# Performance work log

Measured on AMD Instinct MI355X. Metric: run time of the kernel, lower is better.

The kernel has to match this reference:

```python
import jax, jax.numpy as jnp
import numpy as np
import math

DIM = 1024
N_HEADS = 16
HEAD_DIM = DIM // N_HEADS
MAX_LEN = 4096
THETA = 10000.0
LN_EPS = 1e-5


def _rope_tables(dim, max_len, theta=THETA):
    # matches precompute_rope: freqs over even indices, angles = outer(t, freqs)
    inv = 1.0 / theta ** (np.arange(0, dim, 2, dtype=np.float32) / dim)
    t = np.arange(max_len, dtype=np.float32)
    ang = np.outer(t, inv)  # [max_len, dim//2]
    return jnp.asarray(np.cos(ang)), jnp.asarray(np.sin(ang))


def setup_inputs() -> dict:
    key = jax.random.key(0)
    ks = jax.random.split(key, 5)
    B, T, D = 2, 2048, DIM
    s = 1.0 / math.sqrt(D)
    x = jax.random.normal(ks[0], (B, T, D), dtype=jnp.float32)
    wq = jax.random.normal(ks[1], (D, D), dtype=jnp.float32) * s
    wk = jax.random.normal(ks[2], (D, D), dtype=jnp.float32) * s
    wv = jax.random.normal(ks[3], (D, D), dtype=jnp.float32) * s
    wo = jax.random.normal(ks[4], (D, D), dtype=jnp.float32) * s
    ln_g = jnp.ones((D,), dtype=jnp.float32)
    ln_b = jnp.zeros((D,), dtype=jnp.float32)
    cos, sin = _rope_tables(HEAD_DIM, MAX_LEN)
    return {"x": x, "wq": wq, "wk": wk, "wv": wv, "wo": wo,
            "ln_g": ln_g, "ln_b": ln_b, "cos": cos, "sin": sin}


def _rotate(x, cos, sin):
    # x: [B, T, H, hd]; complex multiply on interleaved (even, odd) pairs
    B, T, H, hd = x.shape
    xr = x.reshape(B, T, H, hd // 2, 2)
    x0, x1 = xr[..., 0], xr[..., 1]
    c = cos[None, :T, None, :]
    s = sin[None, :T, None, :]
    o0 = x0 * c - x1 * s
    o1 = x0 * s + x1 * c
    return jnp.stack([o0, o1], axis=-1).reshape(B, T, H, hd)


def reference(x, wq, wk, wv, wo, ln_g, ln_b, cos, sin):
    B, T, D = x.shape
    H, hd = N_HEADS, HEAD_DIM
    # LayerNorm
    mu = jnp.mean(x, axis=-1, keepdims=True)
    var = jnp.var(x, axis=-1, keepdims=True)
    h = (x - mu) * jax.lax.rsqrt(var + LN_EPS) * ln_g + ln_b
    # QKV projections (torch Linear: h @ W.T)
    q = jnp.einsum('btd,ed->bte', h, wq).reshape(B, T, H, hd)
    k = jnp.einsum('btd,ed->bte', h, wk).reshape(B, T, H, hd)
    v = jnp.einsum('btd,ed->bte', h, wv).reshape(B, T, H, hd)
    q = _rotate(q, cos, sin)
    k = _rotate(k, cos, sin)
    # full (non-causal) attention, scores [B, H, T, T]
    scores = jnp.einsum('bqhd,bkhd->bhqk', q, k) / math.sqrt(hd)
    attn = jax.nn.softmax(scores, axis=-1)
    out = jnp.einsum('bhqk,bkhd->bqhd', attn, v).reshape(B, T, D)
    return jnp.einsum('btd,ed->bte', out, wo)
```

## Files before the change

kernel.cpp:

```cpp
#include <hip/hip_runtime.h>
#include <hip/hip_bf16.h>

typedef __attribute__((ext_vector_type(4))) float          fx4;
typedef __attribute__((ext_vector_type(8))) __bf16         bfx8;
typedef __attribute__((ext_vector_type(8))) unsigned short usx8;
typedef __attribute__((ext_vector_type(4))) unsigned short usx4;

#define TLEN 2048
#define ROWS 4096
#define D    1024

__device__ __forceinline__ float bf2f(unsigned short u) {
    union { unsigned int i; float f; } v; v.i = ((unsigned int)u) << 16; return v.f;
}
__device__ __forceinline__ unsigned short f2bf(float f) {
    union { float f; unsigned int i; } v; v.f = f;
    unsigned int r = v.i + 0x7fffu + ((v.i >> 16) & 1u);
    return (unsigned short)(r >> 16);
}
__device__ __forceinline__ unsigned int cvtpk_bf16(float lo, float hi) {
    unsigned int r;
    asm("v_cvt_pk_bf16_f32 %0, %1, %2" : "=v"(r) : "v"(lo), "v"(hi));
    return r;
}
__device__ __forceinline__ void gload_lds16(const unsigned short* g, unsigned short* l) {
    __builtin_amdgcn_global_load_lds((const __attribute__((address_space(1))) void*)g,
                                     (__attribute__((address_space(3))) void*)l, 16, 0, 0);
}

__device__ __forceinline__ usx4 cvt4(fx4 a) {
    usx4 o;
    #pragma unroll
    for (int j = 0; j < 4; j++) o[j] = f2bf(a[j]);
    return o;
}
__global__ __launch_bounds__(256) void prep_kernel(const float* __restrict__ x,
                                                   const float* __restrict__ g,
                                                   const float* __restrict__ bta,
                                                   const float* __restrict__ wq, const float* __restrict__ wk,
                                                   const float* __restrict__ wv, const float* __restrict__ wo,
                                                   unsigned short* __restrict__ hout,
                                                   unsigned short* __restrict__ wqkv,
                                                   unsigned short* __restrict__ wob,
                                                   float* __restrict__ ropeTab) {
    const int tid = threadIdx.x;
    if (blockIdx.x >= 5120) {
        const int idx = (blockIdx.x - 5120) * 256 + tid;
        const int pi_ = idx >> 11, t = idx & 2047;
        float inv = __builtin_amdgcn_exp2f(-0.415241011861f * (float)pi_);
        float ang = (float)t * inv;
        ropeTab[idx * 2]     = cosf(ang);
        ropeTab[idx * 2 + 1] = sinf(ang);
        return;
    }
    if (blockIdx.x >= 4096) {
        const int i = (blockIdx.x - 4096) * 256 + tid;
        ((usx4*)wqkv)[i]          = cvt4(((const fx4*)wq)[i]);
        ((usx4*)wqkv)[262144 + i] = cvt4(((const fx4*)wk)[i]);
        ((usx4*)wqkv)[524288 + i] = cvt4(((const fx4*)wv)[i]);
        ((usx4*)wob)[i]           = cvt4(((const fx4*)wo)[i]);
        return;
    }
    const int row = blockIdx.x;
    fx4 v = ((const fx4*)(x + (size_t)row * D))[tid];
    float s  = v[0] + v[1] + v[2] + v[3];
    float s2 = v[0]*v[0] + v[1]*v[1] + v[2]*v[2] + v[3]*v[3];
    #pragma unroll
    for (int mk = 32; mk >= 1; mk >>= 1) { s += __shfl_xor(s, mk); s2 += __shfl_xor(s2, mk); }
    __shared__ float red[8];
    const int wave = tid >> 6, lane = tid & 63;
    if (lane == 0) { red[wave] = s; red[4 + wave] = s2; }
    __syncthreads();
    s  = red[0] + red[1] + red[2] + red[3];
    s2 = red[4] + red[5] + red[6] + red[7];
    float mu   = s * (1.0f / D);
    float var  = s2 * (1.0f / D) - mu * mu;
    float rstd = rsqrtf(var + 1e-5f);
    fx4 gv = ((const fx4*)g)[tid];
    fx4 bv = ((const fx4*)bta)[tid];
    usx4 o;
    #pragma unroll
    for (int j = 0; j < 4; j++) o[j] = f2bf((v[j] - mu) * rstd * gv[j] + bv[j]);
    ((usx4*)hout)[(size_t)row * 256 + tid] = o;
}

__global__ __launch_bounds__(512) void qkvt_gemm(const unsigned short* __restrict__ hbuf,
                                                 const unsigned short* __restrict__ wqkv,
                                                 unsigned short* __restrict__ qkout,
                                                 unsigned short* __restrict__ vtout,
                                                 const float* __restrict__ ropeTab) {
    constexpr int K = 1024;
    __shared__ __align__(16) unsigned short As[2][256 * 64];
    __shared__ __align__(16) unsigned short Bs[2][256 * 64];
    const int tid = threadIdx.x, lane = tid & 63, wave = tid >> 6;
    const int fr = lane & 15, fq = lane >> 4;
    const int wr = wave >> 2, wc = wave & 3;

    const int id = blockIdx.x;
    const bool isqk = id < 128;
    int bm, bn;
    const unsigned short *Ab, *Bb;
    if (isqk) {
        bm = id & 15; bn = id >> 4;
        Ab = hbuf + (size_t)(bm * 256) * K;
        Bb = wqkv + (size_t)(bn * 256) * K;
    } else {
        int j = id - 128; bm = j & 3; bn = j >> 2;
        Ab = wqkv + (size_t)(2048 * 1024) + (size_t)(bm * 256) * K;
        Bb = hbuf + (size_t)(bn * 256) * K;
    }

    const int srow   = wave * 8 + (lane >> 3);
    const int sc_dst = (lane & 7) * 8;
    const int sc_src = ((lane & 7) ^ (lane >> 3)) * 8;

    #define STAGE_Q(BUF, KT)                                                          \
        {                                                                             \
            _Pragma("unroll")                                                         \
            for (int i = 0; i < 4; i++) {                                             \
                const int r = srow + 64 * i;                                          \
                gload_lds16(Ab + (size_t)r * K + (KT) + sc_src, &As[BUF][r * 64 + sc_dst]); \
                gload_lds16(Bb + (size_t)r * K + (KT) + sc_src, &Bs[BUF][r * 64 + sc_dst]); \
            }                                                                         \
        }

    fx4 acc[8][4];
    #pragma unroll
    for (int m = 0; m < 8; m++)
        #pragma unroll
        for (int n = 0; n < 4; n++) acc[m][n] = (fx4)0.0f;

    STAGE_Q(0, 0)

    for (int kt = 0; kt < K; kt += 64) {
        const int b = (kt >> 6) & 1;
        __syncthreads();
        if (kt + 64 < K) STAGE_Q(b ^ 1, kt + 64)
        #pragma unroll
        for (int s = 0; s < 2; s++) {
            bfx8 aF[8], bF[4];
            #pragma unroll
            for (int m = 0; m < 8; m++)
                aF[m] = *(const bfx8*)&As[b][(wr * 128 + m * 16 + fr) * 64 + (((s * 4 + fq) ^ (fr & 7)) * 8)];
            #pragma unroll
            for (int n = 0; n < 4; n++)
                bF[n] = *(const bfx8*)&Bs[b][(wc * 64 + n * 16 + fr) * 64 + (((s * 4 + fq) ^ (fr & 7)) * 8)];
            #pragma unroll
            for (int m = 0; m < 8; m++)
                #pragma unroll
                for (int n = 0; n < 4; n++)
                    acc[m][n] = __builtin_amdgcn_mfma_f32_16x16x32_bf16(aF[m], bF[n], acc[m][n], 0, 0, 0);
        }
    }
    #undef STAGE_Q

    const int row0 = bm * 256 + wr * 128 + fq * 4;
    const int col0 = bn * 256 + wc * 64 + fr;
    if (isqk) {
        const float QS = 0.125f * 1.44269504088896f;
        const bool isq = bn < 4;
        const float sgn = (fr & 1) ? 1.0f : -1.0f;
        #pragma unroll
        for (int m = 0; m < 8; m++) {
            const int rbase = row0 + m * 16;
            const int tb = rbase & (TLEN - 1);
            #pragma unroll
            for (int n = 0; n < 4; n++) {
                const float* tp = ropeTab + ((((n * 8 + (fr >> 1)) << 11) | tb) << 1);
                fx4 csA = *(const fx4*)tp;
                fx4 csB = *(const fx4*)(tp + 4);
                #pragma unroll
                for (int j = 0; j < 4; j++) {
                    float c  = (j < 2) ? csA[2 * j]     : csB[2 * (j - 2)];
                    float s_ = (j < 2) ? csA[2 * j + 1] : csB[2 * (j - 2) + 1];
                    float self = acc[m][n][j];
                    float other = __shfl_xor(self, 1);
                    float o = self * c + other * (sgn * s_);
                    if (isq) o *= QS;
                    qkout[(size_t)(rbase + j) * 2048 + col0 + n * 16] = f2bf(o);
                }
            }
        }
    } else {
        const int bb = bn >> 3;
        #pragma unroll
        for (int m = 0; m < 8; m++)
            #pragma unroll
            for (int n = 0; n < 4; n++) {
                const int t = (col0 + n * 16) & (TLEN - 1);
                const int tp = (t & ~63) | ((n >> 1) * 32 + ((fr >> 2)) * 8 + ((n & 1)) * 4 + (fr & 3));
                #pragma unroll
                for (int j = 0; j < 4; j++) {
                    const int d = row0 + m * 16 + j;
                    vtout[(((size_t)(bb * 16 + (d >> 6)) * 64) + (d & 63)) * TLEN + tp] = f2bf(acc[m][n][j]);
                }
            }
    }
}

__global__ __launch_bounds__(256) void gemm_out64(const unsigned short* __restrict__ A,
                                                  const unsigned short* __restrict__ B,
                                                  float* __restrict__ C) {
    constexpr int K = 1024;
    __shared__ __align__(16) unsigned short As[128 * 64];
    __shared__ __align__(16) unsigned short Bs[64 * 64];
    const int tid = threadIdx.x, lane = tid & 63, wave = tid >> 6;
    const int fr = lane & 15, fq = lane >> 4;
    const int bm = blockIdx.x, bn = blockIdx.y;
    const int wr = wave >> 1, wc = wave & 1;

    const int srow   = wave * 8 + (lane >> 3);
    const int sc_dst = (lane & 7) * 8;
    const int sc_src = ((lane & 7) ^ (lane >> 3)) * 8;
    const unsigned short* Ab = A + (size_t)(bm * 128) * K;
    const unsigned short* Bb = B + (size_t)(bn * 64) * K;

    fx4 acc[4][2];
    #pragma unroll
    for (int m = 0; m < 4; m++)
        #pragma unroll
        for (int n = 0; n < 2; n++) acc[m][n] = (fx4)0.0f;

    for (int kt = 0; kt < K; kt += 64) {
        #pragma unroll
        for (int i = 0; i < 4; i++) {
            const int r = srow + 32 * i;
            gload_lds16(Ab + (size_t)r * K + kt + sc_src, &As[r * 64 + sc_dst]);
            if (i < 2)
                gload_lds16(Bb + (size_t)r * K + kt + sc_src, &Bs[r * 64 + sc_dst]);
        }
        __syncthreads();
        #pragma unroll
        for (int s = 0; s < 2; s++) {
            bfx8 aF[4], bF[2];
            #pragma unroll
            for (int m = 0; m < 4; m++)
                aF[m] = *(const bfx8*)&As[(wr * 64 + m * 16 + fr) * 64 + (((s * 4 + fq) ^ (fr & 7)) * 8)];
            #pragma unroll
            for (int n = 0; n < 2; n++)
                bF[n] = *(const bfx8*)&Bs[(wc * 32 + n * 16 + fr) * 64 + (((s * 4 + fq) ^ (fr & 7)) * 8)];
            #pragma unroll
            for (int m = 0; m < 4; m++)
                #pragma unroll
                for (int n = 0; n < 2; n++)
                    acc[m][n] = __builtin_amdgcn_mfma_f32_16x16x32_bf16(aF[m], bF[n], acc[m][n], 0, 0, 0);
        }
        __syncthreads();
    }

    const int row0 = bm * 128 + wr * 64 + fq * 4;
    const int col0 = bn * 64 + wc * 32 + fr;
    #pragma unroll
    for (int m = 0; m < 4; m++)
        #pragma unroll
        for (int n = 0; n < 2; n++)
            #pragma unroll
            for (int j = 0; j < 4; j++)
                C[(size_t)(row0 + m * 16 + j) * 1024 + col0 + n * 16] = acc[m][n][j];
}

__global__ __launch_bounds__(512) void attn_kernel(const unsigned short* __restrict__ qk,
                                                   const unsigned short* __restrict__ vt,
                                                   unsigned short* __restrict__ ao) {
    const int flat = blockIdx.x + (blockIdx.y << 3);
    const int sid  = (flat & 7) * 32 + (flat >> 3);
    const int qt = sid & 7, bh = sid >> 3;
    const int b = bh >> 4, hh = bh & 15;
    const int tid = threadIdx.x, lane = tid & 63, wave = tid >> 6;
    const int fr = lane & 15, fq = lane >> 4;

    __shared__ __align__(16) unsigned short sK[2][64 * 64];
    __shared__ __align__(16) unsigned short sVt[2][64 * 64];

    const size_t rs = 2048;
    const unsigned short* qb  = qk + (size_t)b * TLEN * rs + hh * 64;
    const unsigned short* kb  = qb + 1024;
    const unsigned short* vtb = vt + (size_t)bh * (64 * TLEN);

    bfx8 qF[2][2];
    #pragma unroll
    for (int g = 0; g < 2; g++) {
        int qrow = qt * 256 + wave * 32 + g * 16 + fr;
        const unsigned short* qp = qb + (size_t)qrow * rs + fq * 8;
        qF[g][0] = *(const bfx8*)qp;
        qF[g][1] = *(const bfx8*)(qp + 32);
    }
    union { unsigned short us[8]; bfx8 bf; } ones_u;
    #pragma unroll
    for (int i = 0; i < 8; i++) ones_u.us[i] = 0x3F80;

    const int srow = lane >> 3;
    const int scol = ((lane & 7) ^ srow) * 8;

    gload_lds16(kb  + (size_t)(wave * 8 + srow) * rs + scol,   &sK[0][wave * 512 + lane * 8]);
    gload_lds16(vtb + (size_t)(wave * 8 + srow) * TLEN + scol, &sVt[0][wave * 512 + lane * 8]);

    fx4 oacc[2][4];
    fx4 oextra[2] = {(fx4)0.0f, (fx4)0.0f};
    #pragma unroll
    for (int g = 0; g < 2; g++)
        #pragma unroll
        for (int db = 0; db < 4; db++) oacc[g][db] = (fx4)0.0f;

    #pragma unroll 2
    for (int t = 0; t < 32; ++t) {
        const int buf = t & 1;
        __syncthreads();

        if (t + 1 < 32) {
            const int kt = (t + 1) * 64;
            gload_lds16(kb  + (size_t)(kt + wave * 8 + srow) * rs + scol,
                        &sK[buf ^ 1][wave * 512 + lane * 8]);
            gload_lds16(vtb + (size_t)(wave * 8 + srow) * TLEN + kt + scol,
                        &sVt[buf ^ 1][wave * 512 + lane * 8]);
        }

        bfx8 kF[2][4];
        #pragma unroll
        for (int s = 0; s < 2; s++)
            #pragma unroll
            for (int n = 0; n < 4; n++)
                kF[s][n] = *(const bfx8*)&sK[buf][(n * 16 + fr) * 64 + (((s * 4 + fq) ^ (fr & 7)) * 8)];
        fx4 sacc0[4], sacc1[4];
        #pragma unroll
        for (int n = 0; n < 4; n++) { sacc0[n] = (fx4)0.0f; sacc1[n] = (fx4)0.0f; }
        __builtin_amdgcn_s_setprio(1);
        #pragma unroll
        for (int s = 0; s < 2; s++)
            #pragma unroll
            for (int n = 0; n < 4; n++)
                sacc0[n] = __builtin_amdgcn_mfma_f32_16x16x32_bf16(kF[s][n], qF[0][s], sacc0[n], 0, 0, 0);
        #pragma unroll
        for (int s = 0; s < 2; s++)
            #pragma unroll
            for (int n = 0; n < 4; n++)
                sacc1[n] = __builtin_amdgcn_mfma_f32_16x16x32_bf16(kF[s][n], qF[1][s], sacc1[n], 0, 0, 0);
        __builtin_amdgcn_s_setprio(0);

        unsigned int u0[4][2], u1[4][2];
        #pragma unroll
        for (int n = 0; n < 4; n++) {
            u0[n][0] = cvtpk_bf16(__builtin_amdgcn_exp2f(sacc0[n][0]), __builtin_amdgcn_exp2f(sacc0[n][1]));
            u0[n][1] = cvtpk_bf16(__builtin_amdgcn_exp2f(sacc0[n][2]), __builtin_amdgcn_exp2f(sacc0[n][3]));
        }

        bfx8 vF[2][4];
        #pragma unroll
        for (int s = 0; s < 2; s++)
            #pragma unroll
            for (int db = 0; db < 4; db++)
                vF[s][db] = *(const bfx8*)&sVt[buf][(db * 16 + fr) * 64 + (((s * 4 + fq) ^ (fr & 7)) * 8)];

        __builtin_amdgcn_s_setprio(1);
        #pragma unroll
        for (int s = 0; s < 2; s++) {
            union { unsigned int ui[4]; bfx8 bf; } cv;
            cv.ui[0] = u0[2 * s][0];     cv.ui[1] = u0[2 * s][1];
            cv.ui[2] = u0[2 * s + 1][0]; cv.ui[3] = u0[2 * s + 1][1];
            #pragma unroll
            for (int db = 0; db < 4; db++)
                oacc[0][db] = __builtin_amdgcn_mfma_f32_16x16x32_bf16(vF[s][db], cv.bf, oacc[0][db], 0, 0, 0);
            oextra[0] = __builtin_amdgcn_mfma_f32_16x16x32_bf16(ones_u.bf, cv.bf, oextra[0], 0, 0, 0);
        }
        __builtin_amdgcn_s_setprio(0);

        #pragma unroll
        for (int n = 0; n < 4; n++) {
            u1[n][0] = cvtpk_bf16(__builtin_amdgcn_exp2f(sacc1[n][0]), __builtin_amdgcn_exp2f(sacc1[n][1]));
            u1[n][1] = cvtpk_bf16(__builtin_amdgcn_exp2f(sacc1[n][2]), __builtin_amdgcn_exp2f(sacc1[n][3]));
        }

        __builtin_amdgcn_s_setprio(1);
        #pragma unroll
        for (int s = 0; s < 2; s++) {
            union { unsigned int ui[4]; bfx8 bf; } cv;
            cv.ui[0] = u1[2 * s][0];     cv.ui[1] = u1[2 * s][1];
            cv.ui[2] = u1[2 * s + 1][0]; cv.ui[3] = u1[2 * s + 1][1];
            #pragma unroll
            for (int db = 0; db < 4; db++)
                oacc[1][db] = __builtin_amdgcn_mfma_f32_16x16x32_bf16(vF[s][db], cv.bf, oacc[1][db], 0, 0, 0);
            oextra[1] = __builtin_amdgcn_mfma_f32_16x16x32_bf16(ones_u.bf, cv.bf, oextra[1], 0, 0, 0);
        }
        __builtin_amdgcn_s_setprio(0);
    }

    #pragma unroll
    for (int g = 0; g < 2; g++) {
        float invl = 1.0f / oextra[g][0];
        const int qrow = qt * 256 + wave * 32 + g * 16 + fr;
        unsigned short* aop = ao + (size_t)(b * TLEN + qrow) * 1024 + hh * 64 + fq * 4;
        #pragma unroll
        for (int db = 0; db < 4; db++) {
            usx4 o4;
            #pragma unroll
            for (int j = 0; j < 4; j++) o4[j] = f2bf(oacc[g][db][j] * invl);
            *(usx4*)(aop + db * 16) = o4;
        }
    }
}

extern "C" void kernel_launch(void* const* d_in, const int* in_sizes, int n_in,
                              void* d_out, int out_size, void* d_ws, size_t ws_size,
                              hipStream_t stream) {
    const float* x    = (const float*)d_in[0];
    const float* wq   = (const float*)d_in[1];
    const float* wk   = (const float*)d_in[2];
    const float* wv   = (const float*)d_in[3];
    const float* wo   = (const float*)d_in[4];
    const float* lng  = (const float*)d_in[5];
    const float* lnb  = (const float*)d_in[6];

    char* ws = (char*)d_ws;
    unsigned short* wob  = (unsigned short*)(ws);
    unsigned short* wqkv = (unsigned short*)(ws + (2u  << 20));
    unsigned short* hbuf = (unsigned short*)(ws + (8u  << 20));
    unsigned short* qk   = (unsigned short*)(ws + (16u << 20));
    unsigned short* vtb  = (unsigned short*)(ws + (32u << 20));
    unsigned short* ao   = (unsigned short*)(ws + (8u  << 20));
    float* ropeTab = (float*)d_out;

    prep_kernel<<<5632, 256, 0, stream>>>(x, lng, lnb, wq, wk, wv, wo, hbuf, wqkv, wob, ropeTab);
    qkvt_gemm<<<192, 512, 0, stream>>>(hbuf, wqkv, qk, vtb, ropeTab);
    attn_kernel<<<dim3(8, 32), 512, 0, stream>>>(qk, vtb, ao);
    gemm_out64<<<dim3(32, 16), 256, 0, stream>>>(ao, wob, (float*)d_out);
}
```

Baseline: 114.3 us.

## Load QKV GEMM B fragments from global and double attention KV tile size

In the QKV GEMM, the B operand is no longer staged through shared memory. Each wave loads its B fragments directly from global memory into registers, which halves LDS use and the staging traffic. The attention kernel now processes 128 keys per iteration instead of 64, with larger shared buffers, and interleaves K fragment loads with the MFMAs. This halves the number of barriers and loop iterations. The risks are uncoalesced, higher-latency global reads for B that are not covered by prefetching, and higher register and LDS pressure in attention.

```diff
diff --git a/kernel.cpp b/kernel.cpp
--- a/kernel.cpp
+++ b/kernel.cpp
@@ -91,7 +91,6 @@
                                                  const float* __restrict__ ropeTab) {
     constexpr int K = 1024;
     __shared__ __align__(16) unsigned short As[2][256 * 64];
-    __shared__ __align__(16) unsigned short Bs[2][256 * 64];
     const int tid = threadIdx.x, lane = tid & 63, wave = tid >> 6;
     const int fr = lane & 15, fq = lane >> 4;
     const int wr = wave >> 2, wc = wave & 3;
@@ -113,14 +112,14 @@
     const int srow   = wave * 8 + (lane >> 3);
     const int sc_dst = (lane & 7) * 8;
     const int sc_src = ((lane & 7) ^ (lane >> 3)) * 8;
-
-    #define STAGE_Q(BUF, KT)                                                          \
+    const unsigned short* Bfrag = Bb + (size_t)(wc * 64 + fr) * K + fq * 8;
+
+    #define STAGE_A(BUF, KT)                                                          \
         {                                                                             \
             _Pragma("unroll")                                                         \
             for (int i = 0; i < 4; i++) {                                             \
                 const int r = srow + 64 * i;                                          \
                 gload_lds16(Ab + (size_t)r * K + (KT) + sc_src, &As[BUF][r * 64 + sc_dst]); \
-                gload_lds16(Bb + (size_t)r * K + (KT) + sc_src, &Bs[BUF][r * 64 + sc_dst]); \
             }                                                                         \
         }
 
@@ -130,29 +129,33 @@
         #pragma unroll
         for (int n = 0; n < 4; n++) acc[m][n] = (fx4)0.0f;
 
-    STAGE_Q(0, 0)
-
+    STAGE_A(0, 0)
+
+    #pragma unroll 2
     for (int kt = 0; kt < K; kt += 64) {
         const int b = (kt >> 6) & 1;
         __syncthreads();
-        if (kt + 64 < K) STAGE_Q(b ^ 1, kt + 64)
+        if (kt + 64 < K) STAGE_A(b ^ 1, kt + 64)
+        bfx8 bF[2][4];
+        #pragma unroll
+        for (int s = 0; s < 2; s++)
+            #pragma unroll
+            for (int n = 0; n < 4; n++)
+                bF[s][n] = *(const bfx8*)(Bfrag + (size_t)(n * 16) * K + kt + s * 32);
         #pragma unroll
         for (int s = 0; s < 2; s++) {
-            bfx8 aF[8], bF[4];
+            bfx8 aF[8];
             #pragma unroll
             for (int m = 0; m < 8; m++)
                 aF[m] = *(const bfx8*)&As[b][(wr * 128 + m * 16 + fr) * 64 + (((s * 4 + fq) ^ (fr & 7)) * 8)];
-            #pragma unroll
-            for (int n = 0; n < 4; n++)
-                bF[n] = *(const bfx8*)&Bs[b][(wc * 64 + n * 16 + fr) * 64 + (((s * 4 + fq) ^ (fr & 7)) * 8)];
             #pragma unroll
             for (int m = 0; m < 8; m++)
                 #pragma unroll
                 for (int n = 0; n < 4; n++)
-                    acc[m][n] = __builtin_amdgcn_mfma_f32_16x16x32_bf16(aF[m], bF[n], acc[m][n], 0, 0, 0);
-        }
-    }
-    #undef STAGE_Q
+                    acc[m][n] = __builtin_amdgcn_mfma_f32_16x16x32_bf16(aF[m], bF[s][n], acc[m][n], 0, 0, 0);
+        }
+    }
+    #undef STAGE_A
 
     const int row0 = bm * 256 + wr * 128 + fq * 4;
     const int col0 = bn * 256 + wc * 64 + fr;
@@ -269,8 +272,8 @@
     const int tid = threadIdx.x, lane = tid & 63, wave = tid >> 6;
     const int fr = lane & 15, fq = lane >> 4;
 
-    __shared__ __align__(16) unsigned short sK[2][64 * 64];
-    __shared__ __align__(16) unsigned short sVt[2][64 * 64];
+    __shared__ __align__(16) unsigned short sK[2][128 * 64];
+    __shared__ __align__(16) unsigned short sVt[2][2 * 64 * 64];
 
     const size_t rs = 2048;
     const unsigned short* qb  = qk + (size_t)b * TLEN * rs + hh * 64;
@@ -292,8 +295,20 @@
     const int srow = lane >> 3;
     const int scol = ((lane & 7) ^ srow) * 8;
 
-    gload_lds16(kb  + (size_t)(wave * 8 + srow) * rs + scol,   &sK[0][wave * 512 + lane * 8]);
-    gload_lds16(vtb + (size_t)(wave * 8 + srow) * TLEN + scol, &sVt[0][wave * 512 + lane * 8]);
+    #define STAGE_ATTN(BUF, KT)                                                          \
+        {                                                                                \
+            _Pragma("unroll")                                                            \
+            for (int i = 0; i < 2; i++) {                                                \
+                const int rg = wave * 2 + i;                                             \
+                gload_lds16(kb + (size_t)((KT) + rg * 8 + srow) * rs + scol,             \
+                            &sK[BUF][rg * 512 + lane * 8]);                              \
+                const int sub = rg >> 3, drow = (rg & 7) * 8 + srow;                     \
+                gload_lds16(vtb + (size_t)drow * TLEN + (KT) + sub * 64 + scol,          \
+                            &sVt[BUF][rg * 512 + lane * 8]);                             \
+            }                                                                            \
+        }
+
+    STAGE_ATTN(0, 0)
 
     fx4 oacc[2][4];
     fx4 oextra[2] = {(fx4)0.0f, (fx4)0.0f};
@@ -303,86 +318,72 @@
         for (int db = 0; db < 4; db++) oacc[g][db] = (fx4)0.0f;
 
     #pragma unroll 2
-    for (int t = 0; t < 32; ++t) {
+    for (int t = 0; t < 16; ++t) {
         const int buf = t & 1;
         __syncthreads();
 
-        if (t + 1 < 32) {
-            const int kt = (t + 1) * 64;
-            gload_lds16(kb  + (size_t)(kt + wave * 8 + srow) * rs + scol,
-                        &sK[buf ^ 1][wave * 512 + lane * 8]);
-            gload_lds16(vtb + (size_t)(wave * 8 + srow) * TLEN + kt + scol,
-                        &sVt[buf ^ 1][wave * 512 + lane * 8]);
-        }
-
-        bfx8 kF[2][4];
+        if (t + 1 < 16) STAGE_ATTN(buf ^ 1, (t + 1) * 128)
+
+        fx4 s0[8], s1[8];
+        #pragma unroll
+        for (int n = 0; n < 8; n++) { s0[n] = (fx4)0.0f; s1[n] = (fx4)0.0f; }
+        __builtin_amdgcn_s_setprio(1);
         #pragma unroll
         for (int s = 0; s < 2; s++)
             #pragma unroll
-            for (int n = 0; n < 4; n++)
-                kF[s][n] = *(const bfx8*)&sK[buf][(n * 16 + fr) * 64 + (((s * 4 + fq) ^ (fr & 7)) * 8)];
-        fx4 sacc0[4], sacc1[4];
-        #pragma unroll
-        for (int n = 0; n < 4; n++) { sacc0[n] = (fx4)0.0f; sacc1[n] = (fx4)0.0f; }
+            for (int n = 0; n < 8; n++) {
+                bfx8 kF = *(const bfx8*)&sK[buf][(n * 16 + fr) * 64 + (((s * 4 + fq) ^ (fr & 7)) * 8)];
+                s0[n] = __builtin_amdgcn_mfma_f32_16x16x32_bf16(kF, qF[0][s], s0[n], 0, 0, 0);
+                s1[n] = __builtin_amdgcn_mfma_f32_16x16x32_bf16(kF, qF[1][s], s1[n], 0, 0, 0);
+            }
+        __builtin_amdgcn_s_setprio(0);
+
+        unsigned int u0[8][2], u1[8][2];
+        #pragma unroll
+        for (int n = 0; n < 8; n++) {
+            u0[n][0] = cvtpk_bf16(__builtin_amdgcn_exp2f(s0[n][0]), __builtin_amdgcn_exp2f(s0[n][1]));
+            u0[n][1] = cvtpk_bf16(__builtin_amdgcn_exp2f(s0[n][2]), __builtin_amdgcn_exp2f(s0[n][3]));
+        }
+
         __builtin_amdgcn_s_setprio(1);
         #pragma unroll
-        for (int s = 0; s < 2; s++)
-            #pragma unroll
-            for (int n = 0; n < 4; n++)
-                sacc0[n] = __builtin_amdgcn_mfma_f32_16x16x32_bf16(kF[s][n], qF[0][s], sacc0[n], 0, 0, 0);
-        #pragma unroll
-        for (int s = 0; s < 2; s++)
-            #pragma unroll
-            for (int n = 0; n < 4; n++)
-                sacc1[n] = __builtin_amdgcn_mfma_f32_16x16x32_bf16(kF[s][n], qF[1][s], sacc1[n], 0, 0, 0);
+        for (int sp = 0; sp < 4; sp++) {
+            union { unsigned int ui[4]; bfx8 bf; } cv;
+            cv.ui[0] = u0[2 * sp][0];     cv.ui[1] = u0[2 * sp][1];
+            cv.ui[2] = u0[2 * sp + 1][0]; cv.ui[3] = u0[2 * sp + 1][1];
+            #pragma unroll
+            for (int db = 0; db < 4; db++) {
+                bfx8 vF = *(const bfx8*)&sVt[buf][(sp >> 1) * 4096 + (db * 16 + fr) * 64 +
+                                                 ((((sp & 1) * 4 + fq) ^ (fr & 7)) * 8)];
+                oacc[0][db] = __builtin_amdgcn_mfma_f32_16x16x32_bf16(vF, cv.bf, oacc[0][db], 0, 0, 0);
+            }
+            oextra[0] = __builtin_amdgcn_mfma_f32_16x16x32_bf16(ones_u.bf, cv.bf, oextra[0], 0, 0, 0);
+        }
         __builtin_amdgcn_s_setprio(0);
 
-        unsigned int u0[4][2], u1[4][2];
-        #pragma unroll
-        for (int n = 0; n < 4; n++) {
-            u0[n][0] = cvtpk_bf16(__builtin_amdgcn_exp2f(sacc0[n][0]), __builtin_amdgcn_exp2f(sacc0[n][1]));
-            u0[n][1] = cvtpk_bf16(__builtin_amdgcn_exp2f(sacc0[n][2]), __builtin_amdgcn_exp2f(sacc0[n][3]));
-        }
-
-        bfx8 vF[2][4];
-        #pragma unroll
-        for (int s = 0; s < 2; s++)
-            #pragma unroll
-            for (int db = 0; db < 4; db++)
-                vF[s][db] = *(const bfx8*)&sVt[buf][(db * 16 + fr) * 64 + (((s * 4 + fq) ^ (fr & 7)) * 8)];
+        #pragma unroll
+        for (int n = 0; n < 8; n++) {
+            u1[n][0] = cvtpk_bf16(__builtin_amdgcn_exp2f(s1[n][0]), __builtin_amdgcn_exp2f(s1[n][1]));
+            u1[n][1] = cvtpk_bf16(__builtin_amdgcn_exp2f(s1[n][2]), __builtin_amdgcn_exp2f(s1[n][3]));
+        }
 
         __builtin_amdgcn_s_setprio(1);
         #pragma unroll
-        for (int s = 0; s < 2; s++) {
+        for (int sp = 0; sp < 4; sp++) {
             union { unsigned int ui[4]; bfx8 bf; } cv;
-            cv.ui[0] = u0[2 * s][0];     cv.ui[1] = u0[2 * s][1];
-            cv.ui[2] = u0[2 * s + 1][0]; cv.ui[3] = u0[2 * s + 1][1];
-            #pragma unroll
-            for (int db = 0; db < 4; db++)
-                oacc[0][db] = __builtin_amdgcn_mfma_f32_16x16x32_bf16(vF[s][db], cv.bf, oacc[0][db], 0, 0, 0);
-            oextra[0] = __builtin_amdgcn_mfma_f32_16x16x32_bf16(ones_u.bf, cv.bf, oextra[0], 0, 0, 0);
+            cv.ui[0] = u1[2 * sp][0];     cv.ui[1] = u1[2 * sp][1];
+            cv.ui[2] = u1[2 * sp + 1][0]; cv.ui[3] = u1[2 * sp + 1][1];
+            #pragma unroll
+            for (int db = 0; db < 4; db++) {
+                bfx8 vF = *(const bfx8*)&sVt[buf][(sp >> 1) * 4096 + (db * 16 + fr) * 64 +
+                                                 ((((sp & 1) * 4 + fq) ^ (fr & 7)) * 8)];
+                oacc[1][db] = __builtin_amdgcn_mfma_f32_16x16x32_bf16(vF, cv.bf, oacc[1][db], 0, 0, 0);
+            }
+            oextra[1] = __builtin_amdgcn_mfma_f32_16x16x32_bf16(ones_u.bf, cv.bf, oextra[1], 0, 0, 0);
         }
         __builtin_amdgcn_s_setprio(0);
-
-        #pragma unroll
-        for (int n = 0; n < 4; n++) {
-            u1[n][0] = cvtpk_bf16(__builtin_amdgcn_exp2f(sacc1[n][0]), __builtin_amdgcn_exp2f(sacc1[n][1]));
-            u1[n][1] = cvtpk_bf16(__builtin_amdgcn_exp2f(sacc1[n][2]), __builtin_amdgcn_exp2f(sacc1[n][3]));
-        }
-
-        __builtin_amdgcn_s_setprio(1);
-        #pragma unroll
-        for (int s = 0; s < 2; s++) {
-            union { unsigned int ui[4]; bfx8 bf; } cv;
-            cv.ui[0] = u1[2 * s][0];     cv.ui[1] = u1[2 * s][1];
-            cv.ui[2] = u1[2 * s + 1][0]; cv.ui[3] = u1[2 * s + 1][1];
-            #pragma unroll
-            for (int db = 0; db < 4; db++)
-                oacc[1][db] = __builtin_amdgcn_mfma_f32_16x16x32_bf16(vF[s][db], cv.bf, oacc[1][db], 0, 0, 0);
-            oextra[1] = __builtin_amdgcn_mfma_f32_16x16x32_bf16(ones_u.bf, cv.bf, oextra[1], 0, 0, 0);
-        }
-        __builtin_amdgcn_s_setprio(0);
-    }
+    }
+    #undef STAGE_ATTN
 
     #pragma unroll
     for (int g = 0; g < 2; g++) {
```

New measurement: 122.4 us. 1.07x slower.
